# Kernel optimization log

Hardware: AMD Instinct MI355X
Metric: run time of the kernel (lower is better)

The kernel has to match this reference:

```python
import jax, jax.numpy as jnp
import numpy as np

N_NODES = 100000
N_EDGES = 1000000
IN_DIM = 128
OUT_DIM = 64


def setup_inputs() -> dict:
    key = jax.random.key(0)
    k1, k2, k3, k4, k5 = jax.random.split(key, 5)
    X = jax.random.normal(k1, (N_NODES, IN_DIM), dtype=jnp.float32)
    edge_rows = jax.random.randint(k2, (N_EDGES,), 0, N_NODES, dtype=jnp.int64)
    edge_cols = jax.random.randint(k3, (N_EDGES,), 0, N_NODES, dtype=jnp.int64)
    # normalized adjacency values (e.g. 1/sqrt(d_i d_j)), positive and small
    edge_vals = jax.random.uniform(k4, (N_EDGES,), dtype=jnp.float32, minval=0.0, maxval=1.0)
    # xavier-uniform-ish weight
    limit = float(np.sqrt(6.0 / (IN_DIM + OUT_DIM)))
    W = jax.random.uniform(k5, (IN_DIM, OUT_DIM), dtype=jnp.float32, minval=-limit, maxval=limit)
    bias = jnp.zeros((OUT_DIM,), dtype=jnp.float32)
    return {"X": X, "edge_rows": edge_rows, "edge_cols": edge_cols,
            "edge_vals": edge_vals, "W": W, "bias": bias}


def reference(X, edge_rows, edge_cols, edge_vals, W, bias):
    # dense projection: (N, in_dim) @ (in_dim, out_dim) -> (N, out_dim)
    h = X @ W
    # spmm over COO sparse A_norm: out[r] += v * h[c] for each edge (r, c, v)
    msg = edge_vals[:, None] * h[edge_cols]          # (E, out_dim) gather
    agg = jax.ops.segment_sum(msg, edge_rows, num_segments=N_NODES)
    return jax.nn.relu(agg + bias)
```

## Files before the change

kernel.cpp:

```cpp
#include <hip/hip_runtime.h>

#define IN_DIM 128
#define OUT_DIM 64
#define RPB_SHIFT 6
#define RPB 64
#define NBMAX 2048
#define CHUNK 4096
#define SLABCAP 896
#define PADK 136

typedef __attribute__((ext_vector_type(8))) short bf16x8;
typedef __attribute__((ext_vector_type(4))) float f32x4;
typedef __attribute__((ext_vector_type(4))) unsigned short us4;

__device__ inline unsigned short f2bf(float f) {
  unsigned u = __float_as_uint(f);
  u += 0x7FFFu + ((u >> 16) & 1u);
  return (unsigned short)(u >> 16);
}

__global__ __launch_bounds__(256) void zero_int_kernel(int* __restrict__ p, int n) {
  int i = blockIdx.x * 256 + threadIdx.x;
  for (; i < n; i += gridDim.x * 256) p[i] = 0;
}

__global__ __launch_bounds__(512) void fat_kernel(const float* __restrict__ X,
                                                  const float* __restrict__ W,
                                                  unsigned short* __restrict__ H,
                                                  const int* __restrict__ rows,
                                                  const int* __restrict__ cols,
                                                  const float* __restrict__ vals,
                                                  int* __restrict__ cursor,
                                                  uint2* __restrict__ staged,
                                                  int n, int ne, int nb, int nPart) {
  __shared__ __align__(16) unsigned char smem[34816];
  const int t = threadIdx.x;

  if ((int)blockIdx.x < nPart) {
    int* lh    = (int*)smem;
    int* lbase = (int*)(smem + NBMAX * 4);
    const int e0 = blockIdx.x * CHUNK;
    const int e1 = min(e0 + CHUNK, ne);

    for (int i = t; i < nb; i += 512) lh[i] = 0;
    __syncthreads();

    for (int i = e0 + t; i < e1; i += 512)
      atomicAdd(&lh[rows[i] >> RPB_SHIFT], 1);
    __syncthreads();

    for (int i = t; i < nb; i += 512) {
      int c = lh[i];
      lbase[i] = c ? atomicAdd(&cursor[i], c) : 0;
    }
    __syncthreads();
    for (int i = t; i < nb; i += 512) lh[i] = 0;
    __syncthreads();

    for (int i = e0 + t; i < e1; i += 512) {
      int r = rows[i];
      int b = r >> RPB_SHIFT;
      int lofs = atomicAdd(&lh[b], 1);
      int pos = lbase[b] + lofs;
      if (pos < SLABCAP) {
        unsigned key = ((unsigned)(r & (RPB - 1)) << 17) | (unsigned)cols[i];
        staged[(size_t)b * SLABCAP + pos] = make_uint2(key, __float_as_uint(vals[i]));
      }
    }
  } else {
    unsigned short (*Xs)[PADK] = (unsigned short(*)[PADK])smem;
    unsigned short (*Wt)[PADK] = (unsigned short(*)[PADK])(smem + 17408);
    const int lane = t & 63;
    const int wave = t >> 6;
    const int sub = wave & 3;
    const int ch = wave >> 2;
    const int row0 = ((int)blockIdx.x - nPart) * 64;

    {
      const float4* w4 = (const float4*)W;
#pragma unroll
      for (int j = 0; j < 4; ++j) {
        int i4 = t + j * 512;
        int k = i4 >> 4;
        int c = (i4 & 15) * 4;
        float4 v = w4[i4];
        Wt[c + 0][k] = f2bf(v.x);
        Wt[c + 1][k] = f2bf(v.y);
        Wt[c + 2][k] = f2bf(v.z);
        Wt[c + 3][k] = f2bf(v.w);
      }
    }
    {
#pragma unroll
      for (int j = 0; j < 4; ++j) {
        int i4 = t + j * 512;
        int r = i4 >> 5;
        int c4 = i4 & 31;
        int row = row0 + r;
        if (row < n) {
          float4 v = ((const float4*)(X + (size_t)row * IN_DIM))[c4];
          us4 p;
          p.x = f2bf(v.x); p.y = f2bf(v.y); p.z = f2bf(v.z); p.w = f2bf(v.w);
          *(us4*)&Xs[r][c4 * 4] = p;
        }
      }
    }
    __syncthreads();

    f32x4 acc[2] = {};
    const int arow = sub * 16 + (lane & 15);
    const int kg = (lane >> 4) * 8;
#pragma unroll
    for (int kk = 0; kk < 4; ++kk) {
      bf16x8 a = *(const bf16x8*)&Xs[arow][kk * 32 + kg];
#pragma unroll
      for (int nt = 0; nt < 2; ++nt) {
        bf16x8 b = *(const bf16x8*)&Wt[ch * 32 + nt * 16 + (lane & 15)][kk * 32 + kg];
        acc[nt] = __builtin_amdgcn_mfma_f32_16x16x32_bf16(a, b, acc[nt], 0, 0, 0);
      }
    }

    const int orow0 = row0 + sub * 16 + (lane >> 4) * 4;
#pragma unroll
    for (int nt = 0; nt < 2; ++nt) {
      int col = ch * 32 + nt * 16 + (lane & 15);
#pragma unroll
      for (int r = 0; r < 4; ++r) {
        int row = orow0 + r;
        if (row < n) H[(size_t)row * OUT_DIM + col] = f2bf(acc[nt][r]);
      }
    }
  }
}

__global__ __launch_bounds__(512) void spmm_fused_kernel(const int* __restrict__ cursor,
                                                         const uint2* __restrict__ staged,
                                                         const unsigned short* __restrict__ H,
                                                         const float* __restrict__ bias,
                                                         float* __restrict__ out, int n) {
  __shared__ uint2 sorted[SLABCAP];
  __shared__ int rcnt[RPB];
  __shared__ int rstart[RPB];
  __shared__ int rcur[RPB];

  const int b = blockIdx.x;
  const int t = threadIdx.x;
  const int cnt = min(cursor[b], SLABCAP);
  const uint2* slab = staged + (size_t)b * SLABCAP;

  if (t < RPB) rcnt[t] = 0;
  __syncthreads();
  for (int i = t; i < cnt; i += 512) atomicAdd(&rcnt[slab[i].x >> 17], 1);
  __syncthreads();

  if (t < RPB) {
    int v = rcnt[t];
    int x = v;
#pragma unroll
    for (int d = 1; d < RPB; d <<= 1) {
      int y = __shfl_up(x, d);
      if (t >= d) x += y;
    }
    rstart[t] = x - v;
    rcur[t] = x - v;
  }
  __syncthreads();

  for (int i = t; i < cnt; i += 512) {
    uint2 e = slab[i];
    int rl = e.x >> 17;
    int pos = atomicAdd(&rcur[rl], 1);
    sorted[pos] = e;
  }
  __syncthreads();

  const int lane = t & 63;
  const int wave = t >> 6;
  const int q4 = (lane & 15) * 4;
  const float4 bv = *(const float4*)&bias[q4];
  const int row0 = b << RPB_SHIFT;

  for (int rl = wave * 4 + ((lane >> 4) & 3); rl < RPB; rl += 32) {
    const int s = rstart[rl];
    const int c = rcnt[rl];
    float a0 = 0.f, a1 = 0.f, a2 = 0.f, a3 = 0.f;
    int e = 0;
    for (; e + 4 <= c; e += 4) {
      float v[4];
      uint2 hu[4];
#pragma unroll
      for (int k = 0; k < 4; ++k) {
        uint2 en = sorted[s + e + k];
        hu[k] = *(const uint2*)&H[(size_t)(en.x & 0x1FFFF) * OUT_DIM + q4];
        v[k] = __uint_as_float(en.y);
      }
#pragma unroll
      for (int k = 0; k < 4; ++k) {
        a0 = fmaf(v[k], __uint_as_float(hu[k].x << 16), a0);
        a1 = fmaf(v[k], __uint_as_float(hu[k].x & 0xFFFF0000u), a1);
        a2 = fmaf(v[k], __uint_as_float(hu[k].y << 16), a2);
        a3 = fmaf(v[k], __uint_as_float(hu[k].y & 0xFFFF0000u), a3);
      }
    }
    for (; e < c; ++e) {
      uint2 en = sorted[s + e];
      uint2 hu = *(const uint2*)&H[(size_t)(en.x & 0x1FFFF) * OUT_DIM + q4];
      float v = __uint_as_float(en.y);
      a0 = fmaf(v, __uint_as_float(hu.x << 16), a0);
      a1 = fmaf(v, __uint_as_float(hu.x & 0xFFFF0000u), a1);
      a2 = fmaf(v, __uint_as_float(hu.y << 16), a2);
      a3 = fmaf(v, __uint_as_float(hu.y & 0xFFFF0000u), a3);
    }
    int row = row0 + rl;
    if (row < n) {
      float4 o;
      o.x = fmaxf(a0 + bv.x, 0.f);
      o.y = fmaxf(a1 + bv.y, 0.f);
      o.z = fmaxf(a2 + bv.z, 0.f);
      o.w = fmaxf(a3 + bv.w, 0.f);
      *(float4*)(out + (size_t)row * OUT_DIM + q4) = o;
    }
  }
}

extern "C" void kernel_launch(void* const* d_in, const int* in_sizes, int n_in,
                              void* d_out, int out_size, void* d_ws, size_t ws_size,
                              hipStream_t stream) {
  const float* X    = (const float*)d_in[0];
  const int*   rows = (const int*)d_in[1];
  const int*   cols = (const int*)d_in[2];
  const float* vals = (const float*)d_in[3];
  const float* W    = (const float*)d_in[4];
  const float* bias = (const float*)d_in[5];
  float* out = (float*)d_out;

  const int n_nodes = in_sizes[0] / IN_DIM;
  const int n_edges = in_sizes[1];
  const int nb = (n_nodes + RPB - 1) >> RPB_SHIFT;

  char* ws = (char*)d_ws;
  unsigned short* H = (unsigned short*)ws;
  size_t off = (size_t)n_nodes * OUT_DIM * sizeof(unsigned short);
  off = (off + 15) & ~(size_t)15;
  int* cursor  = (int*)(ws + off); off += NBMAX * 4;
  uint2* staged = (uint2*)(ws + off);

  const int nPart = (n_edges + CHUNK - 1) / CHUNK;
  const int nGemm = (n_nodes + 63) / 64;

  zero_int_kernel<<<8, 256, 0, stream>>>(cursor, nb);
  fat_kernel<<<nPart + nGemm, 512, 0, stream>>>(X, W, H, rows, cols, vals, cursor, staged,
                                                n_nodes, n_edges, nb, nPart);
  spmm_fused_kernel<<<nb, 512, 0, stream>>>(cursor, staged, H, bias, out, n_nodes);
}
```

Measured before the change: 64.24 us.

## Precompute bf16 transposed W once and register-cache edge offsets in partition

W is now converted to bf16 and transposed once in a prep kernel that also zeroes the cursors, so each GEMM block reads B fragments straight from global/L2 instead of rebuilding W in LDS. This drops the per-block W conversion and halves LDS use, which may allow more blocks per CU. The partition phase keeps each edge's row and local offset in registers from the first atomic pass. That removes the second histogram reset and the second round of LDS atomics and row reloads. The cost is uncoalesced global reads of WT fragments in the MFMA loop, and a hardcoded assumption that CHUNK equals EPT*512.

```diff
diff --git a/kernel.cpp b/kernel.cpp
--- a/kernel.cpp
+++ b/kernel.cpp
@@ -6,6 +6,7 @@
 #define RPB 64
 #define NBMAX 2048
 #define CHUNK 4096
+#define EPT 8
 #define SLABCAP 896
 #define PADK 136
 
@@ -19,13 +20,27 @@
   return (unsigned short)(u >> 16);
 }
 
-__global__ __launch_bounds__(256) void zero_int_kernel(int* __restrict__ p, int n) {
-  int i = blockIdx.x * 256 + threadIdx.x;
-  for (; i < n; i += gridDim.x * 256) p[i] = 0;
+__global__ __launch_bounds__(256) void prep_kernel(const float* __restrict__ W,
+                                                   unsigned short* __restrict__ WT,
+                                                   int* __restrict__ cursor, int ncur) {
+  const int bid = blockIdx.x, t = threadIdx.x;
+  if (bid < 8) {
+    for (int i = bid * 256 + t; i < ncur; i += 8 * 256) cursor[i] = 0;
+  } else {
+    int gid = (bid - 8) * 256 + t;
+    int c = gid & 63;
+    int kq = gid >> 6;
+    us4 p;
+    p.x = f2bf(W[(4 * kq + 0) * OUT_DIM + c]);
+    p.y = f2bf(W[(4 * kq + 1) * OUT_DIM + c]);
+    p.z = f2bf(W[(4 * kq + 2) * OUT_DIM + c]);
+    p.w = f2bf(W[(4 * kq + 3) * OUT_DIM + c]);
+    *(us4*)(WT + (size_t)c * IN_DIM + 4 * kq) = p;
+  }
 }
 
 __global__ __launch_bounds__(512) void fat_kernel(const float* __restrict__ X,
-                                                  const float* __restrict__ W,
+                                                  const unsigned short* __restrict__ WT,
                                                   unsigned short* __restrict__ H,
                                                   const int* __restrict__ rows,
                                                   const int* __restrict__ cols,
@@ -33,20 +48,29 @@
                                                   int* __restrict__ cursor,
                                                   uint2* __restrict__ staged,
                                                   int n, int ne, int nb, int nPart) {
-  __shared__ __align__(16) unsigned char smem[34816];
+  __shared__ __align__(16) unsigned char smem[17408];
   const int t = threadIdx.x;
 
   if ((int)blockIdx.x < nPart) {
-    int* lh    = (int*)smem;
-    int* lbase = (int*)(smem + NBMAX * 4);
+    int* lh = (int*)smem;
+    int* lbase = lh + NBMAX;
     const int e0 = blockIdx.x * CHUNK;
-    const int e1 = min(e0 + CHUNK, ne);
 
     for (int i = t; i < nb; i += 512) lh[i] = 0;
     __syncthreads();
 
-    for (int i = e0 + t; i < e1; i += 512)
-      atomicAdd(&lh[rows[i] >> RPB_SHIFT], 1);
+    int er[EPT], elofs[EPT];
+#pragma unroll
+    for (int k = 0; k < EPT; ++k) {
+      int i = e0 + t + k * 512;
+      if (i < ne) {
+        int r = rows[i];
+        er[k] = r;
+        elofs[k] = atomicAdd(&lh[r >> RPB_SHIFT], 1);
+      } else {
+        er[k] = -1; elofs[k] = 0;
+      }
+    }
     __syncthreads();
 
     for (int i = t; i < nb; i += 512) {
@@ -54,68 +78,52 @@
       lbase[i] = c ? atomicAdd(&cursor[i], c) : 0;
     }
     __syncthreads();
-    for (int i = t; i < nb; i += 512) lh[i] = 0;
-    __syncthreads();
-
-    for (int i = e0 + t; i < e1; i += 512) {
-      int r = rows[i];
-      int b = r >> RPB_SHIFT;
-      int lofs = atomicAdd(&lh[b], 1);
-      int pos = lbase[b] + lofs;
-      if (pos < SLABCAP) {
-        unsigned key = ((unsigned)(r & (RPB - 1)) << 17) | (unsigned)cols[i];
-        staged[(size_t)b * SLABCAP + pos] = make_uint2(key, __float_as_uint(vals[i]));
+
+#pragma unroll
+    for (int k = 0; k < EPT; ++k) {
+      int i = e0 + t + k * 512;
+      if (er[k] >= 0) {
+        int b = er[k] >> RPB_SHIFT;
+        int pos = lbase[b] + elofs[k];
+        if (pos < SLABCAP) {
+          unsigned key = ((unsigned)(er[k] & (RPB - 1)) << 17) | (unsigned)cols[i];
+          staged[(size_t)b * SLABCAP + pos] = make_uint2(key, __float_as_uint(vals[i]));
+        }
       }
     }
   } else {
     unsigned short (*Xs)[PADK] = (unsigned short(*)[PADK])smem;
-    unsigned short (*Wt)[PADK] = (unsigned short(*)[PADK])(smem + 17408);
     const int lane = t & 63;
     const int wave = t >> 6;
     const int sub = wave & 3;
     const int ch = wave >> 2;
     const int row0 = ((int)blockIdx.x - nPart) * 64;
 
-    {
-      const float4* w4 = (const float4*)W;
-#pragma unroll
-      for (int j = 0; j < 4; ++j) {
-        int i4 = t + j * 512;
-        int k = i4 >> 4;
-        int c = (i4 & 15) * 4;
-        float4 v = w4[i4];
-        Wt[c + 0][k] = f2bf(v.x);
-        Wt[c + 1][k] = f2bf(v.y);
-        Wt[c + 2][k] = f2bf(v.z);
-        Wt[c + 3][k] = f2bf(v.w);
-      }
-    }
-    {
-#pragma unroll
-      for (int j = 0; j < 4; ++j) {
-        int i4 = t + j * 512;
-        int r = i4 >> 5;
-        int c4 = i4 & 31;
-        int row = row0 + r;
-        if (row < n) {
-          float4 v = ((const float4*)(X + (size_t)row * IN_DIM))[c4];
-          us4 p;
-          p.x = f2bf(v.x); p.y = f2bf(v.y); p.z = f2bf(v.z); p.w = f2bf(v.w);
-          *(us4*)&Xs[r][c4 * 4] = p;
-        }
-      }
-    }
-    __syncthreads();
-
+#pragma unroll
+    for (int j = 0; j < 4; ++j) {
+      int i4 = t + j * 512;
+      int r = i4 >> 5;
+      int c4 = i4 & 31;
+      int row = row0 + r;
+      if (row < n) {
+        float4 v = ((const float4*)(X + (size_t)row * IN_DIM))[c4];
+        us4 p;
+        p.x = f2bf(v.x); p.y = f2bf(v.y); p.z = f2bf(v.z); p.w = f2bf(v.w);
+        *(us4*)&Xs[r][c4 * 4] = p;
+      }
+    }
+    __syncthreads();
+
+    const int r16 = lane & 15;
+    const int kg = (lane >> 4) * 8;
     f32x4 acc[2] = {};
-    const int arow = sub * 16 + (lane & 15);
-    const int kg = (lane >> 4) * 8;
 #pragma unroll
     for (int kk = 0; kk < 4; ++kk) {
-      bf16x8 a = *(const bf16x8*)&Xs[arow][kk * 32 + kg];
+      bf16x8 a = *(const bf16x8*)&Xs[sub * 16 + r16][kk * 32 + kg];
 #pragma unroll
       for (int nt = 0; nt < 2; ++nt) {
-        bf16x8 b = *(const bf16x8*)&Wt[ch * 32 + nt * 16 + (lane & 15)][kk * 32 + kg];
+        bf16x8 b = *(const bf16x8*)(WT + (size_t)(ch * 32 + nt * 16 + r16) * IN_DIM
+                                       + kk * 32 + kg);
         acc[nt] = __builtin_amdgcn_mfma_f32_16x16x32_bf16(a, b, acc[nt], 0, 0, 0);
       }
     }
@@ -123,7 +131,7 @@
     const int orow0 = row0 + sub * 16 + (lane >> 4) * 4;
 #pragma unroll
     for (int nt = 0; nt < 2; ++nt) {
-      int col = ch * 32 + nt * 16 + (lane & 15);
+      int col = ch * 32 + nt * 16 + r16;
 #pragma unroll
       for (int r = 0; r < 4; ++r) {
         int row = orow0 + r;
@@ -241,15 +249,18 @@
   char* ws = (char*)d_ws;
   unsigned short* H = (unsigned short*)ws;
   size_t off = (size_t)n_nodes * OUT_DIM * sizeof(unsigned short);
-  off = (off + 15) & ~(size_t)15;
-  int* cursor  = (int*)(ws + off); off += NBMAX * 4;
+  off = (off + 255) & ~(size_t)255;
+  unsigned short* WT = (unsigned short*)(ws + off); off += OUT_DIM * IN_DIM * 2;
+  off = (off + 255) & ~(size_t)255;
+  int* cursor = (int*)(ws + off); off += (size_t)NBMAX * 4;
+  off = (off + 255) & ~(size_t)255;
   uint2* staged = (uint2*)(ws + off);
 
   const int nPart = (n_edges + CHUNK - 1) / CHUNK;
   const int nGemm = (n_nodes + 63) / 64;
 
-  zero_int_kernel<<<8, 256, 0, stream>>>(cursor, nb);
-  fat_kernel<<<nPart + nGemm, 512, 0, stream>>>(X, W, H, rows, cols, vals, cursor, staged,
+  prep_kernel<<<16, 256, 0, stream>>>(W, WT, cursor, nb);
+  fat_kernel<<<nPart + nGemm, 512, 0, stream>>>(X, WT, H, rows, cols, vals, cursor, staged,
                                                 n_nodes, n_edges, nb, nPart);
   spmm_fused_kernel<<<nb, 512, 0, stream>>>(cursor, staged, H, bias, out, n_nodes);
 }
```

New measurement: 70.04 us. 9.0% more time.
